# Kernel tuning notes

Hardware: AMD Instinct MI355X
Metric: run time of the kernel (lower is better)

Reference implementation:

```python
import jax, jax.numpy as jnp
import numpy as np

D_MODEL = 512
NUM_HEADS = 8
DK = D_MODEL // NUM_HEADS
SCALE = DK ** -0.5


def setup_inputs() -> dict:
    key = jax.random.key(0)
    ks = jax.random.split(key, 8)
    B, S = 4, 8192
    q = jax.random.normal(ks[0], (B, S, D_MODEL), dtype=jnp.float32)
    k = jax.random.normal(ks[1], (B, S, D_MODEL), dtype=jnp.float32)
    v = jax.random.normal(ks[2], (B, S, D_MODEL), dtype=jnp.float32)
    init = (2.0 / D_MODEL) ** 0.5  # rough kaiming-like scale
    W_q = jax.random.normal(ks[3], (D_MODEL, D_MODEL), dtype=jnp.float32) * init
    W_k = jax.random.normal(ks[4], (D_MODEL, D_MODEL), dtype=jnp.float32) * init
    W_v = jax.random.normal(ks[5], (D_MODEL, D_MODEL), dtype=jnp.float32) * init
    W_o = jax.random.normal(ks[6], (D_MODEL, D_MODEL), dtype=jnp.float32) * init
    b_o = jax.random.normal(ks[7], (D_MODEL,), dtype=jnp.float32) * 0.01
    return {"q": q, "k": k, "v": v, "W_q": W_q, "W_k": W_k, "W_v": W_v, "W_o": W_o, "b_o": b_o}


def reference(q, k, v, W_q, W_k, W_v, W_o, b_o):
    B, S, C = q.shape
    H, dk = NUM_HEADS, DK
    # projections (torch Linear: x @ W.T)
    qh = (q @ W_q.T).reshape(B, S, H, dk).transpose(0, 2, 1, 3)  # [B,H,S,dk]
    kh = (k @ W_k.T).reshape(B, S, H, dk).transpose(0, 2, 1, 3)
    vh = (v @ W_v.T).reshape(B, S, H, dk).transpose(0, 2, 1, 3)
    # linear attention: G = (K^T * scale) @ V  -> [B,H,dk,dk]
    G = jnp.einsum('bhsd,bhse->bhde', kh * SCALE, vh)
    # out = (Q * scale) @ G  -> [B,H,S,dk]
    out = jnp.einsum('bhsd,bhde->bhse', qh * SCALE, G)
    out = out.transpose(0, 2, 1, 3).reshape(B, S, C)
    return out @ W_o.T + b_o
```

## Files before the change

### kernel.cpp

```cpp
#include <hip/hip_runtime.h>
#include <hip/hip_bf16.h>


typedef __attribute__((ext_vector_type(4))) float f32x4;
typedef __attribute__((ext_vector_type(8))) short short8;

#define DEVI __device__ __forceinline__

DEVI unsigned short f2bf(float f) {
  __bf16 h = (__bf16)f;
  return __builtin_bit_cast(unsigned short, h);
}
DEVI float bf2f(unsigned short s) {
  unsigned int u = ((unsigned int)s) << 16;
  return __builtin_bit_cast(float, u);
}
DEVI short8 pack8(f32x4 a, f32x4 b) {
  short8 r;
#pragma unroll
  for (int i = 0; i < 4; ++i) { r[i] = (short)f2bf(a[i]); r[i + 4] = (short)f2bf(b[i]); }
  return r;
}

__global__ __launch_bounds__(256, 4) void bigm_kernel(const float* __restrict__ kmat,
                                                      const float* __restrict__ vmat,
                                                      unsigned short* __restrict__ Mpart) {
  __shared__ __align__(16) unsigned short Vt[2][128 * 40];
  __shared__ __align__(16) unsigned short Kt[2][128 * 40];
  const int t = threadIdx.x;
  const int bid = blockIdx.x;
  const int xcd = bid & 7, jj = bid >> 3;
  const int p = ((jj >> 4) << 3) | xcd;
  const int tile = jj & 15;
  const int b = p >> 4, split = p & 15;
  const int ti = tile >> 2, tj = tile & 3;
  const int cp0 = ti * 128, ck0 = tj * 128;

  const int lane = t & 63, w = t >> 6;
  const int fr = lane & 15, fg = lane >> 4;
  const int wm = (w >> 1) * 64, wn = (w & 1) * 64;

  const int half = t >> 7;
  const int u = t & 127;
  const int cg = u & 31, sg = u >> 5;
  const float* srcg = (half ? kmat : vmat)
                    + ((size_t)b * 8192 + (size_t)split * 512) * 512
                    + (half ? ck0 : cp0) + cg * 4;
  unsigned short* dstl = (half ? &Kt[0][0] : &Vt[0][0]);
  const int wbase = cg * 4 * 40 + ((sg ^ (cg & 3)) << 3);

  f32x4 r[8];
  auto gload = [&](int sbase) {
    const float* pp = srcg + (size_t)(sbase + sg * 8) * 512;
#pragma unroll
    for (int j = 0; j < 8; ++j) r[j] = *(const f32x4*)(pp + j * 512);
  };
  auto lwrite = [&](int buf) {
    unsigned short* d = dstl + buf * (128 * 40) + wbase;
#pragma unroll
    for (int ci = 0; ci < 4; ++ci) {
      short8 wv;
#pragma unroll
      for (int j = 0; j < 8; ++j) wv[j] = (short)f2bf(r[j][ci]);
      *(short8*)(d + ci * 40) = wv;
    }
  };

  f32x4 acc[4][4] = {};

  gload(0);
  lwrite(0);
  __syncthreads();

  const int key = fr >> 2;
  for (int step = 0; step < 16; ++step) {
    const int cur = step & 1;
    if (step < 15) gload((step + 1) * 32);
    short8 fa[4], fb[4];
#pragma unroll
    for (int i = 0; i < 4; ++i) {
      fa[i] = *(const short8*)&Vt[cur][(wm + i * 16 + fr) * 40 + ((fg ^ key) << 3)];
      fb[i] = *(const short8*)&Kt[cur][(wn + i * 16 + fr) * 40 + ((fg ^ key) << 3)];
    }
#pragma unroll
    for (int i = 0; i < 4; ++i)
#pragma unroll
      for (int j = 0; j < 4; ++j)
        acc[i][j] = __builtin_amdgcn_mfma_f32_16x16x32_bf16(fa[i], fb[j], acc[i][j], 0, 0, 0);
    if (step < 15) lwrite(cur ^ 1);
    __syncthreads();
  }
  unsigned short* gp = Mpart + (size_t)p * 262144;
#pragma unroll
  for (int i = 0; i < 4; ++i)
#pragma unroll
    for (int j = 0; j < 4; ++j)
#pragma unroll
      for (int r2 = 0; r2 < 4; ++r2)
        gp[(size_t)(cp0 + wm + i * 16 + fg * 4 + r2) * 512 + ck0 + wn + j * 16 + fr] =
            f2bf(acc[i][j][r2]);
}

__global__ __launch_bounds__(256) void mred_kernel(const unsigned short* __restrict__ Mpart,
                                                   unsigned short* __restrict__ Msum) {
  const int base = (blockIdx.x * 256 + threadIdx.x) * 8;
  const int b = base >> 18;
  const int r = base & 262143;
  const unsigned short* src = Mpart + (size_t)(b * 16) * 262144 + r;
  float s[8] = {};
#pragma unroll
  for (int c = 0; c < 16; ++c) {
    short8 u = *(const short8*)(src + (size_t)c * 262144);
#pragma unroll
    for (int j = 0; j < 8; ++j) s[j] += bf2f((unsigned short)u[j]);
  }
  short8 o;
#pragma unroll
  for (int j = 0; j < 8; ++j) o[j] = (short)f2bf(s[j]);
  *(short8*)(Msum + base) = o;
}

__global__ __launch_bounds__(256, 3) void stepa_kernel(const float* __restrict__ Wk,
                                                       const unsigned short* __restrict__ Msum,
                                                       unsigned short* __restrict__ P) {
  __shared__ __align__(16) unsigned short Ab[2][128 * 40];
  __shared__ __align__(16) unsigned short Bb[2][128 * 40];
  const int t = threadIdx.x;
  const int n0 = blockIdx.x * 128;
  const int m0 = blockIdx.y * 128;
  const int b = blockIdx.z;
  const int lane = t & 63, w = t >> 6;
  const int wm = (w >> 1) * 64, wn = (w & 1) * 64;
  const int fr = lane & 15, fg = lane >> 4;
  const int sr = t >> 2;
  const int sk = (t & 3) * 8;

  const float* pAg = Wk + (size_t)(m0 + sr) * 512 + sk;
  const unsigned short* pBg = Msum + (size_t)b * 262144 + (size_t)(n0 + sr) * 512 + sk;

  f32x4 acc[4][4] = {};
  f32x4 a0, a1, a2, a3;
  short8 sb0, sb1;

  a0 = *(const f32x4*)(pAg);         a1 = *(const f32x4*)(pAg + 4);
  a2 = *(const f32x4*)(pAg + 32768); a3 = *(const f32x4*)(pAg + 32772);
  sb0 = *(const short8*)(pBg);
  sb1 = *(const short8*)(pBg + 32768);
  *(short8*)&Ab[0][sr * 40 + sk] = pack8(a0, a1);
  *(short8*)&Ab[0][(sr + 64) * 40 + sk] = pack8(a2, a3);
  *(short8*)&Bb[0][sr * 40 + sk] = sb0;
  *(short8*)&Bb[0][(sr + 64) * 40 + sk] = sb1;
  __syncthreads();

  for (int step = 0; step < 16; ++step) {
    const int cur = step & 1;
    if (step < 15) {
      const int k1 = (step + 1) * 32;
      a0 = *(const f32x4*)(pAg + k1);         a1 = *(const f32x4*)(pAg + k1 + 4);
      a2 = *(const f32x4*)(pAg + k1 + 32768); a3 = *(const f32x4*)(pAg + k1 + 32772);
      sb0 = *(const short8*)(pBg + k1);
      sb1 = *(const short8*)(pBg + k1 + 32768);
    }
    short8 afr[4], bfr[4];
#pragma unroll
    for (int i = 0; i < 4; ++i) {
      afr[i] = *(const short8*)&Ab[cur][(wm + i * 16 + fr) * 40 + fg * 8];
      bfr[i] = *(const short8*)&Bb[cur][(wn + i * 16 + fr) * 40 + fg * 8];
    }
#pragma unroll
    for (int i = 0; i < 4; ++i)
#pragma unroll
      for (int j = 0; j < 4; ++j)
        acc[i][j] = __builtin_amdgcn_mfma_f32_16x16x32_bf16(afr[i], bfr[j], acc[i][j], 0, 0, 0);
    if (step < 15) {
      const int nxt = cur ^ 1;
      *(short8*)&Ab[nxt][sr * 40 + sk] = pack8(a0, a1);
      *(short8*)&Ab[nxt][(sr + 64) * 40 + sk] = pack8(a2, a3);
      *(short8*)&Bb[nxt][sr * 40 + sk] = sb0;
      *(short8*)&Bb[nxt][(sr + 64) * 40 + sk] = sb1;
    }
    __syncthreads();
  }
#pragma unroll
  for (int i = 0; i < 4; ++i)
#pragma unroll
    for (int j = 0; j < 4; ++j)
#pragma unroll
      for (int r = 0; r < 4; ++r) {
        const int row = m0 + wm + i * 16 + fg * 4 + r;
        const int col = n0 + wn + j * 16 + fr;
        P[((size_t)b * 512 + row) * 512 + col] = f2bf(acc[i][j][r]);
      }
}

__global__ __launch_bounds__(64) void stepb_kernel(const unsigned short* __restrict__ P,
                                                   const float* __restrict__ Wv,
                                                   float* __restrict__ Gsum) {
  __shared__ __align__(16) unsigned short Ao[64 * 40];
  __shared__ __align__(16) unsigned short Bo[64 * 40];
  const int t = threadIdx.x;
  const int h = blockIdx.x;
  const int b = blockIdx.y;
  const int fr = t & 15, fg = t >> 4;
  f32x4 acc[4][4] = {};
  for (int step = 0; step < 16; ++step) {
    const int k0 = step * 32;
    const unsigned short* pa = P + ((size_t)b * 512 + h * 64 + t) * 512 + k0;
#pragma unroll
    for (int i = 0; i < 4; ++i) *(short8*)&Ao[t * 40 + i * 8] = *(const short8*)(pa + i * 8);
    const float* pb = Wv + (size_t)(h * 64 + t) * 512 + k0;
#pragma unroll
    for (int i = 0; i < 4; ++i) {
      f32x4 x0 = *(const f32x4*)(pb + i * 8);
      f32x4 x1 = *(const f32x4*)(pb + i * 8 + 4);
      *(short8*)&Bo[t * 40 + i * 8] = pack8(x0, x1);
    }
    __syncthreads();
    short8 afr[4], bfr[4];
#pragma unroll
    for (int i = 0; i < 4; ++i) {
      afr[i] = *(const short8*)&Ao[(i * 16 + fr) * 40 + fg * 8];
      bfr[i] = *(const short8*)&Bo[(i * 16 + fr) * 40 + fg * 8];
    }
#pragma unroll
    for (int i = 0; i < 4; ++i)
#pragma unroll
      for (int j = 0; j < 4; ++j)
        acc[i][j] = __builtin_amdgcn_mfma_f32_16x16x32_bf16(afr[i], bfr[j], acc[i][j], 0, 0, 0);
    __syncthreads();
  }
  float* gout = Gsum + (size_t)(b * 8 + h) * 4096;
#pragma unroll
  for (int i = 0; i < 4; ++i)
#pragma unroll
    for (int j = 0; j < 4; ++j)
#pragma unroll
      for (int r = 0; r < 4; ++r)
        gout[(i * 16 + fg * 4 + r) * 64 + (j * 16 + fr)] = acc[i][j][r] * 0.015625f;
}

__global__ __launch_bounds__(256) void t3_kernel(const float* __restrict__ Wq,
                                                 const float* __restrict__ Gsum,
                                                 unsigned short* __restrict__ T3) {
  __shared__ float Wl[64][64];
  __shared__ float Gl[64][64];
  const int t = threadIdx.x;
  const int c0 = blockIdx.x * 64;
  const int h = blockIdx.y;
  const int b = blockIdx.z;
  const int dd = t >> 2;
  const int c4 = (t & 3) * 16;
  const float* wp = Wq + (size_t)(h * 64 + dd) * 512 + c0 + c4;
  const float* gp = Gsum + (size_t)(b * 8 + h) * 4096 + dd * 64 + c4;
#pragma unroll
  for (int i = 0; i < 4; ++i) {
    *(f32x4*)&Wl[dd][c4 + i * 4] = *(const f32x4*)(wp + i * 4);
    *(f32x4*)&Gl[dd][c4 + i * 4] = *(const f32x4*)(gp + i * 4);
  }
  __syncthreads();
  const int cl0 = (t >> 4) * 4;
  const int e0 = (t & 15) * 4;
  float acc[4][4] = {};
  for (int d = 0; d < 64; ++d) {
    f32x4 wv = *(const f32x4*)&Wl[d][cl0];
    f32x4 gv = *(const f32x4*)&Gl[d][e0];
#pragma unroll
    for (int i = 0; i < 4; ++i)
#pragma unroll
      for (int j = 0; j < 4; ++j)
        acc[i][j] += wv[i] * gv[j];
  }
#pragma unroll
  for (int i = 0; i < 4; ++i)
#pragma unroll
    for (int j = 0; j < 4; ++j)
      T3[((size_t)b * 512 + c0 + cl0 + i) * 512 + h * 64 + e0 + j] = f2bf(acc[i][j]);
}

__global__ __launch_bounds__(64) void wc_kernel(const float* __restrict__ Wo,
                                                const unsigned short* __restrict__ T3,
                                                unsigned short* __restrict__ WcT) {
  __shared__ __align__(16) unsigned short Ao[64 * 48];
  __shared__ __align__(16) unsigned short Bo[64 * 48];
  const int t = threadIdx.x;
  const int n0 = blockIdx.x * 64;
  const int c0 = blockIdx.y * 64;
  const int b = blockIdx.z;
  const int fr = t & 15, fg = t >> 4;
  f32x4 acc[4][4] = {};
  for (int step = 0; step < 16; ++step) {
    const int k0 = step * 32;
    const float* pa = Wo + (size_t)(n0 + t) * 512 + k0;
    unsigned short tmp[32];
#pragma unroll
    for (int i = 0; i < 8; ++i) {
      f32x4 vv = *(const f32x4*)(pa + i * 4);
#pragma unroll
      for (int j = 0; j < 4; ++j) tmp[i * 4 + j] = f2bf(vv[j]);
    }
#pragma unroll
    for (int i = 0; i < 4; ++i) *(short8*)&Ao[t * 48 + i * 8] = *(const short8*)&tmp[i * 8];
    const unsigned short* pb = T3 + ((size_t)b * 512 + c0 + t) * 512 + k0;
#pragma unroll
    for (int i = 0; i < 4; ++i) *(short8*)&Bo[t * 48 + i * 8] = *(const short8*)(pb + i * 8);
    __syncthreads();
    short8 afr[4], bfr[4];
#pragma unroll
    for (int i = 0; i < 4; ++i) {
      afr[i] = *(const short8*)&Ao[(i * 16 + fr) * 48 + fg * 8];
      bfr[i] = *(const short8*)&Bo[(i * 16 + fr) * 48 + fg * 8];
    }
#pragma unroll
    for (int i = 0; i < 4; ++i)
#pragma unroll
      for (int j = 0; j < 4; ++j)
        acc[i][j] = __builtin_amdgcn_mfma_f32_16x16x32_bf16(afr[i], bfr[j], acc[i][j], 0, 0, 0);
    __syncthreads();
  }
#pragma unroll
  for (int i = 0; i < 4; ++i)
#pragma unroll
    for (int j = 0; j < 4; ++j)
#pragma unroll
      for (int r = 0; r < 4; ++r)
        WcT[((size_t)b * 512 + n0 + i * 16 + fg * 4 + r) * 512 + c0 + j * 16 + fr] =
            f2bf(acc[i][j][r]);
}

__global__ __launch_bounds__(256, 3) void out_kernel(const float* __restrict__ q,
                                                     const unsigned short* __restrict__ WcT,
                                                     const float* __restrict__ bo,
                                                     float* __restrict__ Out) {
  __shared__ __align__(16) unsigned short Ab[2][128 * 40];
  __shared__ __align__(16) unsigned short Bb[2][128 * 40];
  const int t = threadIdx.x;
  const int bid = blockIdx.x;
  const int xcd = bid & 7, idx = bid >> 3;
  const int mt = xcd * 32 + (idx >> 2);
  const int nt = idx & 3;
  const int m0 = mt * 128, n0 = nt * 128;
  const unsigned short* Wc = WcT + ((size_t)(m0 >> 13)) * 512 * 512;
  const int lane = t & 63, w = t >> 6;
  const int wm = (w >> 1) * 64, wn = (w & 1) * 64;
  const int fr = lane & 15, fg = lane >> 4;
  const int sr = t >> 2;
  const int sk = (t & 3) * 8;

  const float* pAg = q + (size_t)(m0 + sr) * 512 + sk;
  const unsigned short* pBg = Wc + (size_t)(n0 + sr) * 512 + sk;

  f32x4 aA[4], aB[4];
  short8 bA[2], bB[2];
  auto gloadA = [&](int k) {
    aA[0] = *(const f32x4*)(pAg + k);         aA[1] = *(const f32x4*)(pAg + k + 4);
    aA[2] = *(const f32x4*)(pAg + k + 32768); aA[3] = *(const f32x4*)(pAg + k + 32772);
    bA[0] = *(const short8*)(pBg + k);
    bA[1] = *(const short8*)(pBg + k + 32768);
  };
  auto gloadB = [&](int k) {
    aB[0] = *(const f32x4*)(pAg + k);         aB[1] = *(const f32x4*)(pAg + k + 4);
    aB[2] = *(const f32x4*)(pAg + k + 32768); aB[3] = *(const f32x4*)(pAg + k + 32772);
    bB[0] = *(const short8*)(pBg + k);
    bB[1] = *(const short8*)(pBg + k + 32768);
  };
  auto lwriteA = [&](int buf) {
    *(short8*)&Ab[buf][sr * 40 + sk] = pack8(aA[0], aA[1]);
    *(short8*)&Ab[buf][(sr + 64) * 40 + sk] = pack8(aA[2], aA[3]);
    *(short8*)&Bb[buf][sr * 40 + sk] = bA[0];
    *(short8*)&Bb[buf][(sr + 64) * 40 + sk] = bA[1];
  };
  auto lwriteB = [&](int buf) {
    *(short8*)&Ab[buf][sr * 40 + sk] = pack8(aB[0], aB[1]);
    *(short8*)&Ab[buf][(sr + 64) * 40 + sk] = pack8(aB[2], aB[3]);
    *(short8*)&Bb[buf][sr * 40 + sk] = bB[0];
    *(short8*)&Bb[buf][(sr + 64) * 40 + sk] = bB[1];
  };

  f32x4 acc[4][4] = {};
  auto mfma_phase = [&](int cbuf) {
    short8 afr[4], bfr[4];
#pragma unroll
    for (int i = 0; i < 4; ++i) {
      afr[i] = *(const short8*)&Ab[cbuf][(wm + i * 16 + fr) * 40 + fg * 8];
      bfr[i] = *(const short8*)&Bb[cbuf][(wn + i * 16 + fr) * 40 + fg * 8];
    }
#pragma unroll
    for (int i = 0; i < 4; ++i)
#pragma unroll
      for (int j = 0; j < 4; ++j)
        acc[i][j] = __builtin_amdgcn_mfma_f32_16x16x32_bf16(afr[i], bfr[j], acc[i][j], 0, 0, 0);
  };

  gloadA(0);
  lwriteA(0);
  gloadB(32);
  __syncthreads();

  for (int it = 0; it < 8; ++it) {
    const int s0 = it * 2;
    if (it < 7) gloadA((s0 + 2) * 32);
    mfma_phase(0);
    lwriteB(1);
    __syncthreads();
    if (it < 7) gloadB((s0 + 3) * 32);
    mfma_phase(1);
    if (it < 7) lwriteA(0);
    __syncthreads();
  }

  float bias[4];
#pragma unroll
  for (int j = 0; j < 4; ++j) bias[j] = bo[n0 + wn + j * 16 + fr];
#pragma unroll
  for (int i = 0; i < 4; ++i)
#pragma unroll
    for (int j = 0; j < 4; ++j)
#pragma unroll
      for (int r = 0; r < 4; ++r) {
        const int row = m0 + wm + i * 16 + fg * 4 + r;
        const int col = n0 + wn + j * 16 + fr;
        Out[(size_t)row * 512 + col] = acc[i][j][r] + bias[j];
      }
}

extern "C" void kernel_launch(void* const* d_in, const int* in_sizes, int n_in,
                              void* d_out, int out_size, void* d_ws, size_t ws_size,
                              hipStream_t stream) {
  const float* q  = (const float*)d_in[0];
  const float* k  = (const float*)d_in[1];
  const float* v  = (const float*)d_in[2];
  const float* Wq = (const float*)d_in[3];
  const float* Wk = (const float*)d_in[4];
  const float* Wv = (const float*)d_in[5];
  const float* Wo = (const float*)d_in[6];
  const float* bo = (const float*)d_in[7];
  float* Out = (float*)d_out;

  unsigned short* Mpart = (unsigned short*)d_out;
  char* ws = (char*)d_ws;
  unsigned short* Msum = (unsigned short*)ws;
  unsigned short* P    = (unsigned short*)(ws + (size_t)2 * 1048576);
  float* Gsum          = (float*)(ws + (size_t)4 * 1048576);
  unsigned short* T3   = (unsigned short*)(ws + (size_t)5 * 1048576);
  unsigned short* WcT  = (unsigned short*)(ws + (size_t)7 * 1048576);

  bigm_kernel<<<1024, 256, 0, stream>>>(k, v, Mpart);
  mred_kernel<<<512, 256, 0, stream>>>(Mpart, Msum);
  stepa_kernel<<<dim3(4, 4, 4), 256, 0, stream>>>(Wk, Msum, P);
  stepb_kernel<<<dim3(8, 4), 64, 0, stream>>>(P, Wv, Gsum);
  t3_kernel<<<dim3(8, 8, 4), 256, 0, stream>>>(Wq, Gsum, T3);
  wc_kernel<<<dim3(8, 8, 4), 64, 0, stream>>>(Wo, T3, WcT);
  out_kernel<<<1024, 256, 0, stream>>>(q, WcT, bo, Out);
}
```

Baseline: 158.1 us.

## Widen bigm tile to 128x256 to halve redundant V loads

The k^T·v Gram partial kernel now computes 128x256 output tiles per block instead of 128x128, with each wave holding a 64x128 accumulator, and the grid is halved to 512 blocks. Each V column slice is reused across twice as many K columns, which cuts the repeated global reads of the fp32 V input and the bf16 conversion work. The cost is higher register pressure (32 accumulators per wave, with the min-occupancy launch bound removed), more LDS per block, and fewer blocks to hide latency.

```diff
diff --git a/kernel.cpp b/kernel.cpp
--- a/kernel.cpp
+++ b/kernel.cpp
@@ -2,6 +2,7 @@
 #include <hip/hip_bf16.h>
 
 
+typedef __attribute__((ext_vector_type(2))) float f32x2;
 typedef __attribute__((ext_vector_type(4))) float f32x4;
 typedef __attribute__((ext_vector_type(8))) short short8;
 
@@ -22,51 +23,61 @@
   return r;
 }
 
-__global__ __launch_bounds__(256, 4) void bigm_kernel(const float* __restrict__ kmat,
-                                                      const float* __restrict__ vmat,
-                                                      unsigned short* __restrict__ Mpart) {
+__global__ __launch_bounds__(256) void bigm_kernel(const float* __restrict__ kmat,
+                                                   const float* __restrict__ vmat,
+                                                   unsigned short* __restrict__ Mpart) {
   __shared__ __align__(16) unsigned short Vt[2][128 * 40];
-  __shared__ __align__(16) unsigned short Kt[2][128 * 40];
+  __shared__ __align__(16) unsigned short Kt[2][256 * 40];
   const int t = threadIdx.x;
   const int bid = blockIdx.x;
   const int xcd = bid & 7, jj = bid >> 3;
-  const int p = ((jj >> 4) << 3) | xcd;
-  const int tile = jj & 15;
+  const int p = ((jj >> 3) << 3) | xcd;
+  const int tile = jj & 7;
   const int b = p >> 4, split = p & 15;
-  const int ti = tile >> 2, tj = tile & 3;
-  const int cp0 = ti * 128, ck0 = tj * 128;
+  const int ti = tile >> 1, tj = tile & 1;
+  const int cp0 = ti * 128, ck0 = tj * 256;
 
   const int lane = t & 63, w = t >> 6;
   const int fr = lane & 15, fg = lane >> 4;
-  const int wm = (w >> 1) * 64, wn = (w & 1) * 64;
-
-  const int half = t >> 7;
-  const int u = t & 127;
-  const int cg = u & 31, sg = u >> 5;
-  const float* srcg = (half ? kmat : vmat)
-                    + ((size_t)b * 8192 + (size_t)split * 512) * 512
-                    + (half ? ck0 : cp0) + cg * 4;
-  unsigned short* dstl = (half ? &Kt[0][0] : &Vt[0][0]);
-  const int wbase = cg * 4 * 40 + ((sg ^ (cg & 3)) << 3);
-
-  f32x4 r[8];
-  auto gload = [&](int sbase) {
-    const float* pp = srcg + (size_t)(sbase + sg * 8) * 512;
-#pragma unroll
-    for (int j = 0; j < 8; ++j) r[j] = *(const f32x4*)(pp + j * 512);
+  const int wm = (w >> 1) * 64, wn = (w & 1) * 128;
+
+  const size_t sbase0 = ((size_t)b * 8192 + (size_t)split * 512) * 512;
+
+  const int acg = t >> 2, asg = t & 3;
+  const float* srcA = vmat + sbase0 + (size_t)(asg * 8) * 512 + cp0 + acg * 2;
+  const int bcg = t >> 2, bsg = t & 3;
+  const float* srcB = kmat + sbase0 + (size_t)(bsg * 8) * 512 + ck0 + bcg * 4;
+
+  f32x2 ra[8];
+  f32x4 rb[8];
+  auto gload = [&](int s0) {
+    const float* pa = srcA + (size_t)s0 * 512;
+    const float* pb = srcB + (size_t)s0 * 512;
+#pragma unroll
+    for (int j = 0; j < 8; ++j) ra[j] = *(const f32x2*)(pa + j * 512);
+#pragma unroll
+    for (int j = 0; j < 8; ++j) rb[j] = *(const f32x4*)(pb + j * 512);
   };
   auto lwrite = [&](int buf) {
-    unsigned short* d = dstl + buf * (128 * 40) + wbase;
+    unsigned short* da = &Vt[buf][0];
+#pragma unroll
+    for (int ci = 0; ci < 2; ++ci) {
+      short8 wv;
+#pragma unroll
+      for (int j = 0; j < 8; ++j) wv[j] = (short)f2bf(ra[j][ci]);
+      *(short8*)(da + (acg * 2 + ci) * 40 + ((asg ^ ((acg >> 1) & 3)) << 3)) = wv;
+    }
+    unsigned short* db = &Kt[buf][0];
 #pragma unroll
     for (int ci = 0; ci < 4; ++ci) {
       short8 wv;
 #pragma unroll
-      for (int j = 0; j < 8; ++j) wv[j] = (short)f2bf(r[j][ci]);
-      *(short8*)(d + ci * 40) = wv;
-    }
-  };
-
-  f32x4 acc[4][4] = {};
+      for (int j = 0; j < 8; ++j) wv[j] = (short)f2bf(rb[j][ci]);
+      *(short8*)(db + (bcg * 4 + ci) * 40 + ((bsg ^ (bcg & 3)) << 3)) = wv;
+    }
+  };
+
+  f32x4 acc[4][8] = {};
 
   gload(0);
   lwrite(0);
@@ -76,16 +87,17 @@
   for (int step = 0; step < 16; ++step) {
     const int cur = step & 1;
     if (step < 15) gload((step + 1) * 32);
-    short8 fa[4], fb[4];
-#pragma unroll
-    for (int i = 0; i < 4; ++i) {
+    short8 fa[4], fb[8];
+#pragma unroll
+    for (int i = 0; i < 4; ++i)
       fa[i] = *(const short8*)&Vt[cur][(wm + i * 16 + fr) * 40 + ((fg ^ key) << 3)];
-      fb[i] = *(const short8*)&Kt[cur][(wn + i * 16 + fr) * 40 + ((fg ^ key) << 3)];
-    }
-#pragma unroll
-    for (int i = 0; i < 4; ++i)
-#pragma unroll
-      for (int j = 0; j < 4; ++j)
+#pragma unroll
+    for (int j = 0; j < 8; ++j)
+      fb[j] = *(const short8*)&Kt[cur][(wn + j * 16 + fr) * 40 + ((fg ^ key) << 3)];
+#pragma unroll
+    for (int i = 0; i < 4; ++i)
+#pragma unroll
+      for (int j = 0; j < 8; ++j)
         acc[i][j] = __builtin_amdgcn_mfma_f32_16x16x32_bf16(fa[i], fb[j], acc[i][j], 0, 0, 0);
     if (step < 15) lwrite(cur ^ 1);
     __syncthreads();
@@ -94,7 +106,7 @@
 #pragma unroll
   for (int i = 0; i < 4; ++i)
 #pragma unroll
-    for (int j = 0; j < 4; ++j)
+    for (int j = 0; j < 8; ++j)
 #pragma unroll
       for (int r2 = 0; r2 < 4; ++r2)
         gp[(size_t)(cp0 + wm + i * 16 + fg * 4 + r2) * 512 + ck0 + wn + j * 16 + fr] =
@@ -444,7 +456,7 @@
   unsigned short* T3   = (unsigned short*)(ws + (size_t)5 * 1048576);
   unsigned short* WcT  = (unsigned short*)(ws + (size_t)7 * 1048576);
 
-  bigm_kernel<<<1024, 256, 0, stream>>>(k, v, Mpart);
+  bigm_kernel<<<512, 256, 0, stream>>>(k, v, Mpart);
   mred_kernel<<<512, 256, 0, stream>>>(Mpart, Msum);
   stepa_kernel<<<dim3(4, 4, 4), 256, 0, stream>>>(Wk, Msum, P);
   stepb_kernel<<<dim3(8, 4), 64, 0, stream>>>(P, Wv, Gsum);
```

Result: slower. 209.5 us (+32.5%).
